# Optimization experiments

Measured on AMD Instinct MI355X. Metric: run time of the kernel, lower is better.

The kernel has to match this reference:

```python
import jax, jax.numpy as jnp
import numpy as np
import math

N_FREQ = 10
N_FRAGMENTS = 4_000_000
CELL_N = 2000
GENE_N = 1000
EMB_DIM = N_FREQ * 2 * 2  # 40


def setup_inputs() -> dict:
    key = jax.random.key(0)
    k1, k2, k3, k4 = jax.random.split(key, 4)
    coords = jax.random.normal(k1, (N_FRAGMENTS, 2), dtype=jnp.float32)
    ix = jnp.sort(jax.random.randint(k2, (N_FRAGMENTS,), 0, CELL_N * GENE_N, dtype=jnp.int32))
    # buffers, exactly as in FragmentEmbedder.__init__
    freqs = np.array([[1.0 / 100.0 ** (2.0 * i / N_FREQ)] * 2 for i in range(1, N_FREQ + 1)],
                     dtype=np.float32).reshape(-1)  # [2*n_freq]
    shifts = np.array([[0.0, math.pi / 2.0] for _ in range(1, N_FREQ + 1)],
                      dtype=np.float32).reshape(-1)  # [2*n_freq]
    # params (weight1 is zero-init in the original; use small random so output is non-trivial)
    weight1 = jax.random.normal(k3, (1, EMB_DIM), dtype=jnp.float32) * 0.02
    bias1 = jax.random.normal(k4, (GENE_N,), dtype=jnp.float32)  # mean_gene_expression
    return {
        "fragment_coordinates": coords,
        "fragment_cellxgene_ix": ix,
        "cell_n": CELL_N,
        "gene_n": GENE_N,
        "gene_ix": jnp.arange(GENE_N, dtype=jnp.int32),
        "frequencies": jnp.asarray(freqs),
        "shifts": jnp.asarray(shifts),
        "weight1": weight1,
        "bias1": bias1,
    }


def reference(fragment_coordinates, fragment_cellxgene_ix, cell_n, gene_n, gene_ix,
              frequencies, shifts, weight1, bias1):
    F = fragment_coordinates.shape[0]
    # sinusoidal fragment embedding: [F, 2, 2*n_freq] -> [F, 4*n_freq]
    emb = jnp.sin(fragment_coordinates[..., None] * frequencies + shifts).reshape(F, -1)
    # sorted segment sum into cell x gene buckets
    pooled = jax.ops.segment_sum(emb, fragment_cellxgene_ix,
                                 num_segments=cell_n * gene_n,
                                 indices_are_sorted=True)
    cell_gene_embedding = pooled.reshape(cell_n, gene_n, emb.shape[-1])
    # einsum 'abc,bc->ab' with weight1 of shape (1, C) == contraction over C only
    expression = jnp.einsum("abc,c->ab", cell_gene_embedding, weight1[0]) + bias1[gene_ix]
    return expression
```

## Files before the change

kernel.cpp:

```cpp
#include <hip/hip_runtime.h>
#include <math.h>

#define NFREQ 10
#define INV2PI 0.15915494309189535f
#define TPB 256

typedef float v2f __attribute__((ext_vector_type(2)));

__device__ float g_fr[NFREQ];
__device__ v2f   g_P[NFREQ];
__device__ v2f   g_R[NFREQ];

__device__ __forceinline__ v2f mkv2(float a, float b) { v2f r; r.x = a; r.y = b; return r; }

__global__ void coeff_kernel(const float* __restrict__ freqs,
                             const float* __restrict__ weight) {
    int i = threadIdx.x;
    if (i < NFREQ) {
        g_fr[i] = freqs[2 * i] * INV2PI;
        float A0 = weight[2 * i],             B0 = weight[2 * i + 1];
        float A1 = weight[2 * NFREQ + 2 * i], B1 = weight[2 * NFREQ + 2 * i + 1];
        g_R[i] = mkv2(sqrtf(A0 * A0 + B0 * B0), sqrtf(A1 * A1 + B1 * B1));
        g_P[i] = mkv2(atan2f(B0, A0) * INV2PI, atan2f(B1, A1) * INV2PI);
    }
}

__device__ __forceinline__ float frag_eval(v2f c, const float* __restrict__ fr,
                                           const v2f* __restrict__ P,
                                           const v2f* __restrict__ R) {
    v2f acc = mkv2(0.f, 0.f);
#pragma unroll
    for (int i = 0; i < NFREQ; ++i) {
        v2f th = c * fr[i] + P[i];
        v2f s;
        s.x = __builtin_amdgcn_sinf(th.x);
        s.y = __builtin_amdgcn_sinf(th.y);
        acc += R[i] * s;
    }
    return acc.x + acc.y;
}

__global__ __launch_bounds__(TPB) void scan_kernel(
        const float* __restrict__ coords,
        const int*   __restrict__ ix,
        const float* __restrict__ bias,
        const int*   __restrict__ gix,
        float* __restrict__ out,
        int gene_n, int total, int F) {
    float fr[NFREQ]; v2f P[NFREQ], R[NFREQ];
#pragma unroll
    for (int i = 0; i < NFREQ; ++i) {
        fr[i] = g_fr[i]; P[i] = g_P[i]; R[i] = g_R[i];
    }

    const int w    = (blockIdx.x * TPB + threadIdx.x) >> 6;
    const int lane = threadIdx.x & 63;
    const int b    = w << 7;
    if (b >= F) return;
    const int e  = min(b + 128, F);
    const int pk = (b > 0) ? ix[b - 1] : -1;
    const int nk = (e < F) ? ix[e] : 0x7fffffff;
    const int lk = ix[e - 1];

    const int f0 = b + 2 * lane;
    int   ka = -2, kb = -2;
    float sa = 0.f, sb = 0.f;
    if (f0 + 1 < F) {
        int2   k2 = *(const int2*)(ix + f0);
        float4 c4 = *(const float4*)(coords + 2 * f0);
        ka = k2.x; kb = k2.y;
        sa = frag_eval(mkv2(c4.x, c4.y), fr, P, R);
        sb = frag_eval(mkv2(c4.z, c4.w), fr, P, R);
    } else if (f0 < F) {
        ka = kb = ix[f0];
        float2 c2 = *(const float2*)(coords + 2 * f0);
        sa = frag_eval(mkv2(c2.x, c2.y), fr, P, R);
    }

    const bool pure = (ka == kb);
    float v = pure ? (sa + sb) : sa;
#pragma unroll
    for (int d = 1; d < 64; d <<= 1) {
        float ov = __shfl_down(v, d);
        int   ok = __shfl_down(ka, d);
        if (lane + d < 64 && ok == ka) v += ov;
    }
    const float nv  = __shfl_down(v, 1);
    const int   nkl = __shfl_down(ka, 1);
    const int   pkb = __shfl_up(kb, 1);

    if (ka >= 0 && (lane == 0 || ka != pkb)) {
        const int Pk = (lane == 0) ? pk : pkb;
        for (int K2 = Pk + 1; K2 < ka; ++K2)
            out[K2] = bias[gix[K2 % gene_n]];
        if (!(ka == lk && lk == nk)) {
            float tot = v;
            if (lane == 0 && ka == pk) {
                for (int j = b - 1; j >= 0 && ix[j] == ka; --j) {
                    float2 c2 = *(const float2*)(coords + 2 * j);
                    tot += frag_eval(mkv2(c2.x, c2.y), fr, P, R);
                }
            }
            out[ka] = bias[gix[ka % gene_n]] + tot;
        }
    }
    if (kb >= 0 && kb != ka) {
        for (int K2 = ka + 1; K2 < kb; ++K2)
            out[K2] = bias[gix[K2 % gene_n]];
        if (!(kb == lk && lk == nk)) {
            float tb = sb + ((lane < 63 && nkl == kb) ? nv : 0.f);
            out[kb] = bias[gix[kb % gene_n]] + tb;
        }
    }
    if (e == F && lane == 0) {
        for (int K2 = lk + 1; K2 < total; ++K2)
            out[K2] = bias[gix[K2 % gene_n]];
    }
}

extern "C" void kernel_launch(void* const* d_in, const int* in_sizes, int n_in,
                              void* d_out, int out_size, void* d_ws, size_t ws_size,
                              hipStream_t stream) {
    const float* coords  = (const float*)d_in[0];
    const int*   ix      = (const int*)d_in[1];
    const int*   gene_ix = (const int*)d_in[4];
    const float* freqs   = (const float*)d_in[5];
    const float* weight  = (const float*)d_in[7];
    const float* bias    = (const float*)d_in[8];
    float* out = (float*)d_out;

    int F      = in_sizes[1];
    int gene_n = in_sizes[4];
    int total  = out_size;

    (void)d_ws; (void)ws_size; (void)n_in;

    hipLaunchKernelGGL(coeff_kernel, dim3(1), dim3(64), 0, stream,
                       freqs, weight);

    int blocks = (F + TPB * 2 - 1) / (TPB * 2);
    hipLaunchKernelGGL(scan_kernel, dim3(blocks), dim3(TPB), 0, stream,
                       coords, ix, bias, gene_ix, out, gene_n, total, F);
}
```

Baseline: 122.7 us.

## Split bias fill into a separate vectorized kernel and accumulate segments on top

A new fill kernel writes bias values over the whole output with float4 stores and also computes the per-frequency coefficients. The scan kernel then only adds segment sums into out, instead of writing the gaps between keys with serial per-lane loops. The backward walk for a segment that starts in an earlier chunk becomes wave-parallel with a reduction, replacing a single-lane serial loop. This adds a full output write and read-modify-write traffic in exchange for removing divergent scalar gap-fill loops. Only the owning chunk adds each segment's value, so plain += without atomics avoids races.

Measured after the change: 116.2 us. 1.06x faster.

```diff
diff --git a/kernel.cpp b/kernel.cpp
--- a/kernel.cpp
+++ b/kernel.cpp
@@ -13,15 +13,33 @@
 
 __device__ __forceinline__ v2f mkv2(float a, float b) { v2f r; r.x = a; r.y = b; return r; }
 
-__global__ void coeff_kernel(const float* __restrict__ freqs,
-                             const float* __restrict__ weight) {
-    int i = threadIdx.x;
-    if (i < NFREQ) {
+__global__ __launch_bounds__(256) void fill_kernel(
+        float* __restrict__ out, const float* __restrict__ bias,
+        const int* __restrict__ gix, int gene_n, int total, double inv_g,
+        const float* __restrict__ freqs, const float* __restrict__ weight) {
+    if (blockIdx.x == 0 && threadIdx.x < NFREQ) {
+        int i = threadIdx.x;
         g_fr[i] = freqs[2 * i] * INV2PI;
         float A0 = weight[2 * i],             B0 = weight[2 * i + 1];
         float A1 = weight[2 * NFREQ + 2 * i], B1 = weight[2 * NFREQ + 2 * i + 1];
         g_R[i] = mkv2(sqrtf(A0 * A0 + B0 * B0), sqrtf(A1 * A1 + B1 * B1));
         g_P[i] = mkv2(atan2f(B0, A0) * INV2PI, atan2f(B1, A1) * INV2PI);
+    }
+    int b = (blockIdx.x * 256 + threadIdx.x) * 4;
+    if (b >= total) return;
+    int q = (int)((b + 0.5) * inv_g);
+    int g = b - q * gene_n;
+    float v[4];
+#pragma unroll
+    for (int k = 0; k < 4; ++k) {
+        int gg = g + k;
+        if (gg >= gene_n) gg -= gene_n;
+        v[k] = bias[gix[gg]];
+    }
+    if (b + 3 < total) {
+        *(float4*)(out + b) = make_float4(v[0], v[1], v[2], v[3]);
+    } else {
+        for (int k = 0; k < 4 && b + k < total; ++k) out[b + k] = v[k];
     }
 }
 
@@ -43,10 +61,8 @@
 __global__ __launch_bounds__(TPB) void scan_kernel(
         const float* __restrict__ coords,
         const int*   __restrict__ ix,
-        const float* __restrict__ bias,
-        const int*   __restrict__ gix,
         float* __restrict__ out,
-        int gene_n, int total, int F) {
+        int F) {
     float fr[NFREQ]; v2f P[NFREQ], R[NFREQ];
 #pragma unroll
     for (int i = 0; i < NFREQ; ++i) {
@@ -89,32 +105,34 @@
     const int   nkl = __shfl_down(ka, 1);
     const int   pkb = __shfl_up(kb, 1);
 
+    const int  ka0   = __shfl(ka, 0);
+    const bool ends0 = !(ka0 == lk && lk == nk);
+    if (pk == ka0 && ends0) {
+        float wb = 0.f;
+        int j = b - 1 - lane;
+        for (;;) {
+            bool m = (j >= 0) && (ix[j] == ka0);
+            if (m) {
+                float2 c2 = *(const float2*)(coords + 2 * j);
+                wb += frag_eval(mkv2(c2.x, c2.y), fr, P, R);
+            }
+            if (!__all(m)) break;
+            j -= 64;
+        }
+#pragma unroll
+        for (int d = 1; d < 64; d <<= 1) wb += __shfl_xor(wb, d);
+        if (lane == 0) v += wb;
+    }
+
     if (ka >= 0 && (lane == 0 || ka != pkb)) {
-        const int Pk = (lane == 0) ? pk : pkb;
-        for (int K2 = Pk + 1; K2 < ka; ++K2)
-            out[K2] = bias[gix[K2 % gene_n]];
-        if (!(ka == lk && lk == nk)) {
-            float tot = v;
-            if (lane == 0 && ka == pk) {
-                for (int j = b - 1; j >= 0 && ix[j] == ka; --j) {
-                    float2 c2 = *(const float2*)(coords + 2 * j);
-                    tot += frag_eval(mkv2(c2.x, c2.y), fr, P, R);
-                }
-            }
-            out[ka] = bias[gix[ka % gene_n]] + tot;
-        }
+        if (!(ka == lk && lk == nk))
+            out[ka] += v;
     }
     if (kb >= 0 && kb != ka) {
-        for (int K2 = ka + 1; K2 < kb; ++K2)
-            out[K2] = bias[gix[K2 % gene_n]];
         if (!(kb == lk && lk == nk)) {
             float tb = sb + ((lane < 63 && nkl == kb) ? nv : 0.f);
-            out[kb] = bias[gix[kb % gene_n]] + tb;
+            out[kb] += tb;
         }
-    }
-    if (e == F && lane == 0) {
-        for (int K2 = lk + 1; K2 < total; ++K2)
-            out[K2] = bias[gix[K2 % gene_n]];
     }
 }
 
@@ -135,10 +153,12 @@
 
     (void)d_ws; (void)ws_size; (void)n_in;
 
-    hipLaunchKernelGGL(coeff_kernel, dim3(1), dim3(64), 0, stream,
-                       freqs, weight);
+    int fthreads = (total + 3) / 4;
+    hipLaunchKernelGGL(fill_kernel, dim3((fthreads + 255) / 256), dim3(256),
+                       0, stream, out, bias, gene_ix, gene_n, total,
+                       1.0 / (double)gene_n, freqs, weight);
 
     int blocks = (F + TPB * 2 - 1) / (TPB * 2);
     hipLaunchKernelGGL(scan_kernel, dim3(blocks), dim3(TPB), 0, stream,
-                       coords, ix, bias, gene_ix, out, gene_n, total, F);
+                       coords, ix, out, F);
 }
```
